# Performance work log

Measured on AMD Instinct MI355X. Metric: run time of the kernel, lower is better.

## Reference

```python
import jax, jax.numpy as jnp
import numpy as np
from functools import partial

H = 1024  # hidden_sz
B, T = 32, 256
NL = 4    # stacked LSTM layers
WSCALE = 0.02


def setup_inputs() -> dict:
    key = jax.random.key(0)
    ks = jax.random.split(key, 8)
    x = jax.random.normal(ks[0], (B, T, H), dtype=jnp.float32)
    h0 = jnp.zeros((B, H), dtype=jnp.float32)
    c0 = jnp.zeros((B, H), dtype=jnp.float32)
    # LSTM params per layer: kernel [H,4H], recurrent kernel [H,4H], bias [4H]
    Wk = jax.random.normal(ks[1], (NL, H, 4 * H), dtype=jnp.float32) * WSCALE
    Wr = jax.random.normal(ks[2], (NL, H, 4 * H), dtype=jnp.float32) * WSCALE
    b = jnp.zeros((NL, 4 * H), dtype=jnp.float32)
    # dense head
    Wd = jax.random.normal(ks[3], (H, H), dtype=jnp.float32) * WSCALE
    bd = jnp.zeros((H,), dtype=jnp.float32)
    return {"x": x, "h0": h0, "c0": c0, "Wk": Wk, "Wr": Wr, "b": b, "Wd": Wd, "bd": bd}


def _lstm_layer(x_tbd, h0, c0, Wk, Wr, b):
    # Keras LSTM with activation='relu', recurrent_activation='sigmoid'.
    # Gate order in keras kernels: i, f, c(candidate), o.
    xw = jnp.einsum('tbd,dg->tbg', x_tbd, Wk) + b  # precompute input projections [T,B,4H]

    def step(carry, xw_t):
        h, c = carry
        z = xw_t + h @ Wr  # [B,4H]
        i, f, g, o = jnp.split(z, 4, axis=-1)
        i = jax.nn.sigmoid(i)
        f = jax.nn.sigmoid(f)
        o = jax.nn.sigmoid(o)
        c = f * c + i * jax.nn.relu(g)
        h = o * jax.nn.relu(c)
        return (h, c), h

    (hT, cT), hs = jax.lax.scan(step, (h0, c0), xw)
    return hs, hT, cT  # hs: [T,B,H]


def reference(x, h0, c0, Wk, Wr, b, Wd, bd):
    # x: [B,T,H] -> time-major [T,B,H]
    seq = jnp.transpose(x, (1, 0, 2))
    h, c = h0, c0
    for l in range(NL):
        seq, h, c = _lstm_layer(seq, h, c, Wk[l], Wr[l], b[l])
        # dropout layers are identity at inference (training=False)
    out = jnp.einsum('tbh,hd->tbd', seq, Wd) + bd
    out = jnp.transpose(out, (1, 0, 2))  # back to [B,T,H]
    return out, h, c
```

## Files before the change

### kernel.cpp

```cpp
#include <hip/hip_runtime.h>

#define TT 256
#define BB 32
#define HH 1024
#define GG 4096

__global__ __launch_bounds__(256) void k_transpose(const float* __restrict__ x, float* __restrict__ seq) {
    int idx = blockIdx.x * 256 + threadIdx.x;
    int k4 = idx & 255;
    int tb = idx >> 8;
    int t = tb >> 5, b = tb & 31;
    float4 v = ((const float4*)x)[((size_t)b * TT + t) * 256 + k4];
    ((float4*)seq)[(size_t)tb * 256 + k4] = v;
}

__global__ __launch_bounds__(256) void k_init_hc(const float* __restrict__ h0, const float* __restrict__ c0,
                                                 float* __restrict__ h, float* __restrict__ c) {
    int i = blockIdx.x * 256 + threadIdx.x;
    ((float4*)h)[i] = ((const float4*)h0)[i];
    ((float4*)c)[i] = ((const float4*)c0)[i];
}

__global__ __launch_bounds__(256) void k_copy_hc(const float* __restrict__ h, const float* __restrict__ c,
                                                 float* __restrict__ oh, float* __restrict__ oc) {
    int i = blockIdx.x * 256 + threadIdx.x;
    ((float4*)oh)[i] = ((const float4*)h)[i];
    ((float4*)oc)[i] = ((const float4*)c)[i];
}

__global__ __launch_bounds__(256) void k_wrt(const float* __restrict__ Wr, float* __restrict__ WrT) {
    __shared__ float tile[64][65];
    int c0 = blockIdx.x * 64;
    int k0 = blockIdx.y * 64;
    int tid = threadIdx.x;
    int tr = tid >> 4, tc4 = tid & 15;
#pragma unroll
    for (int p = 0; p < 4; ++p) {
        int r = p * 16 + tr;
        float4 v = *(const float4*)&Wr[(size_t)(k0 + r) * GG + c0 + tc4 * 4];
        tile[r][tc4 * 4 + 0] = v.x;
        tile[r][tc4 * 4 + 1] = v.y;
        tile[r][tc4 * 4 + 2] = v.z;
        tile[r][tc4 * 4 + 3] = v.w;
    }
    __syncthreads();
#pragma unroll
    for (int p = 0; p < 4; ++p) {
        int cc = p * 16 + tr;
        float4 v;
        v.x = tile[tc4 * 4 + 0][cc];
        v.y = tile[tc4 * 4 + 1][cc];
        v.z = tile[tc4 * 4 + 2][cc];
        v.w = tile[tc4 * 4 + 3][cc];
        *(float4*)&WrT[(size_t)(c0 + cc) * 1024 + k0 + tc4 * 4] = v;
    }
}

template <int MODE>
__global__ __launch_bounds__(256) void k_gemm(const float* __restrict__ A, const float* __restrict__ W,
                                              const float* __restrict__ bias, float* __restrict__ C, int N) {
    __shared__ float As[16][132];
    __shared__ float Bs[16][132];
    const int K = 1024;
    int tid = threadIdx.x;
    int m0 = blockIdx.x * 128, n0 = blockIdx.y * 128;
    int tx = tid & 15, ty = tid >> 4;
    int a_row = tid >> 2, a_kq = tid & 3;
    int b_cq = tid & 31, b_k = tid >> 5;
    float acc[8][8];
#pragma unroll
    for (int i = 0; i < 8; ++i)
#pragma unroll
        for (int jj = 0; jj < 8; ++jj) acc[i][jj] = 0.f;

    for (int kc = 0; kc < K; kc += 16) {
#pragma unroll
        for (int it = 0; it < 2; ++it) {
            int row = a_row + it * 64;
            float4 v = *(const float4*)&A[(size_t)(m0 + row) * K + kc + a_kq * 4];
            As[a_kq * 4 + 0][row] = v.x;
            As[a_kq * 4 + 1][row] = v.y;
            As[a_kq * 4 + 2][row] = v.z;
            As[a_kq * 4 + 3][row] = v.w;
        }
#pragma unroll
        for (int it = 0; it < 2; ++it) {
            int kk = b_k + it * 8;
            float4 v = *(const float4*)&W[(size_t)(kc + kk) * N + n0 + b_cq * 4];
            *(float4*)&Bs[kk][b_cq * 4] = v;
        }
        __syncthreads();
#pragma unroll
        for (int kk = 0; kk < 16; ++kk) {
            float4 a0 = *(const float4*)&As[kk][ty * 8];
            float4 a1 = *(const float4*)&As[kk][ty * 8 + 4];
            float4 b0 = *(const float4*)&Bs[kk][tx * 8];
            float4 b1 = *(const float4*)&Bs[kk][tx * 8 + 4];
            float am[8] = {a0.x, a0.y, a0.z, a0.w, a1.x, a1.y, a1.z, a1.w};
            float bv[8] = {b0.x, b0.y, b0.z, b0.w, b1.x, b1.y, b1.z, b1.w};
#pragma unroll
            for (int i = 0; i < 8; ++i)
#pragma unroll
                for (int jj = 0; jj < 8; ++jj) acc[i][jj] += am[i] * bv[jj];
        }
        __syncthreads();
    }
#pragma unroll
    for (int i = 0; i < 8; ++i) {
        int m = m0 + ty * 8 + i;
#pragma unroll
        for (int jj = 0; jj < 8; jj += 4) {
            int n = n0 + tx * 8 + jj;
            float4 v;
            v.x = acc[i][jj + 0] + bias[n + 0];
            v.y = acc[i][jj + 1] + bias[n + 1];
            v.z = acc[i][jj + 2] + bias[n + 2];
            v.w = acc[i][jj + 3] + bias[n + 3];
            if (MODE == 0) {
                *(float4*)&C[(size_t)m * N + n] = v;
            } else {
                int t = m >> 5, b = m & 31;
                *(float4*)&C[((size_t)b * TT + t) * HH + n] = v;
            }
        }
    }
}

__global__ __launch_bounds__(512) void k_step_T3(const float* __restrict__ WrT, const float* __restrict__ xw_t,
                                                 float* __restrict__ seq_t, const float* __restrict__ h_in,
                                                 float* __restrict__ h_out, float* __restrict__ c) {
    __shared__ float h_lds[34816];
    __shared__ float zred[8][32][17];
    int tid = threadIdx.x;
    int j = tid & 15, ks = tid >> 4;
    int hc0 = blockIdx.x * 4;
    int col = (j >> 2) * HH + hc0 + (j & 3);

    const float4* WrT4 = (const float4*)WrT;
    int wbase = col * 256 + ks * 8;
    float4 w[8];
#pragma unroll
    for (int q = 0; q < 8; ++q) w[q] = WrT4[wbase + q];

    int rb = tid >> 2, rd = tid & 3;
    float pz[4];
    if (tid < 128) {
#pragma unroll
        for (int g = 0; g < 4; ++g) pz[g] = xw_t[rb * GG + g * HH + hc0 + rd];
    }

    const float4* hp4 = (const float4*)h_in;
    float4* hl4w = (float4*)h_lds;
#pragma unroll 8
    for (int it = 0; it < 16; ++it) {
        int gi = it * 512 + tid;
        float4 v = hp4[gi];
        int b = gi >> 8, kk = gi & 255;
        hl4w[b * 272 + (kk >> 4) * 17 + (kk & 15)] = v;
    }
    __syncthreads();

    const float4* hl4 = (const float4*)h_lds;
    int base4 = (ks >> 1) * 17 + (ks & 1) * 8;
    float acc[32];
#pragma unroll
    for (int b = 0; b < 32; ++b) acc[b] = 0.f;
#pragma unroll
    for (int q = 0; q < 8; ++q) {
        float4 wq = w[q];
#pragma unroll
        for (int b = 0; b < 32; ++b) {
            float4 hv = hl4[b * 272 + base4 + q];
            acc[b] += wq.x * hv.x + wq.y * hv.y + wq.z * hv.z + wq.w * hv.w;
        }
    }
#pragma unroll
    for (int b = 0; b < 32; ++b) {
        acc[b] += __shfl_xor(acc[b], 16);
        acc[b] += __shfl_xor(acc[b], 32);
    }
    int wv = tid >> 6;
    if ((ks & 3) == 0) {
#pragma unroll
        for (int b = 0; b < 32; ++b) zred[wv][b][j] = acc[b];
    }
    __syncthreads();

    if (tid < 128) {
        float zz[4];
#pragma unroll
        for (int g = 0; g < 4; ++g) {
            float s = pz[g];
#pragma unroll
            for (int u = 0; u < 8; ++u) s += zred[u][rb][g * 4 + rd];
            zz[g] = s;
        }
        float si = 1.f / (1.f + expf(-zz[0]));
        float sf = 1.f / (1.f + expf(-zz[1]));
        float gg = fmaxf(zz[2], 0.f);
        float so = 1.f / (1.f + expf(-zz[3]));
        float cv = c[rb * HH + hc0 + rd];
        cv = sf * cv + si * gg;
        c[rb * HH + hc0 + rd] = cv;
        float hn = so * fmaxf(cv, 0.f);
        h_out[rb * HH + hc0 + rd] = hn;
        seq_t[rb * HH + hc0 + rd] = hn;
    }
}

__global__ __launch_bounds__(256) void k_step(const float* __restrict__ Wr, const float* __restrict__ xw_t,
                                              float* __restrict__ seq_t, const float* __restrict__ h_in,
                                              float* __restrict__ h_out, float* __restrict__ c) {
    __shared__ float zred[4][32][17];
    int tid = threadIdx.x;
    int j = tid & 15, ks = tid >> 4;
    int hc0 = blockIdx.x * 4;
    int col = (j >> 2) * HH + hc0 + (j & 3);
    float4 w[16];
#pragma unroll
    for (int q = 0; q < 16; ++q) {
        size_t kb = (size_t)(ks * 64 + q * 4) * GG + col;
        w[q].x = Wr[kb];
        w[q].y = Wr[kb + GG];
        w[q].z = Wr[kb + 2 * (size_t)GG];
        w[q].w = Wr[kb + 3 * (size_t)GG];
    }
    const float4* hp = (const float4*)h_in;
    int kq0 = ks * 16;
    float acc[32];
#pragma unroll
    for (int b = 0; b < 32; ++b) acc[b] = 0.f;
#pragma unroll
    for (int q = 0; q < 16; ++q) {
        float4 wq = w[q];
#pragma unroll
        for (int b = 0; b < 32; ++b) {
            float4 hv = hp[b * 256 + kq0 + q];
            acc[b] += wq.x * hv.x + wq.y * hv.y + wq.z * hv.z + wq.w * hv.w;
        }
    }
#pragma unroll
    for (int b = 0; b < 32; ++b) {
        acc[b] += __shfl_xor(acc[b], 16);
        acc[b] += __shfl_xor(acc[b], 32);
    }
    int wv = tid >> 6;
    if ((ks & 3) == 0) {
#pragma unroll
        for (int b = 0; b < 32; ++b) zred[wv][b][j] = acc[b];
    }
    __syncthreads();
    if (tid < 128) {
        int rb = tid >> 2, rd = tid & 3;
        float zz[4];
#pragma unroll
        for (int g = 0; g < 4; ++g) {
            float s = xw_t[rb * GG + g * HH + hc0 + rd];
#pragma unroll
            for (int u = 0; u < 4; ++u) s += zred[u][rb][g * 4 + rd];
            zz[g] = s;
        }
        float si = 1.f / (1.f + expf(-zz[0]));
        float sf = 1.f / (1.f + expf(-zz[1]));
        float gg = fmaxf(zz[2], 0.f);
        float so = 1.f / (1.f + expf(-zz[3]));
        float cv = c[rb * HH + hc0 + rd];
        cv = sf * cv + si * gg;
        c[rb * HH + hc0 + rd] = cv;
        float hn = so * fmaxf(cv, 0.f);
        h_out[rb * HH + hc0 + rd] = hn;
        seq_t[rb * HH + hc0 + rd] = hn;
    }
}

extern "C" void kernel_launch(void* const* d_in, const int* in_sizes, int n_in,
                              void* d_out, int out_size, void* d_ws, size_t ws_size,
                              hipStream_t stream) {
    const float* x  = (const float*)d_in[0];
    const float* h0 = (const float*)d_in[1];
    const float* c0 = (const float*)d_in[2];
    const float* Wk = (const float*)d_in[3];
    const float* Wr = (const float*)d_in[4];
    const float* bs = (const float*)d_in[5];
    const float* Wd = (const float*)d_in[6];
    const float* bd = (const float*)d_in[7];
    float* out = (float*)d_out;
    float* ws  = (float*)d_ws;

    float* xw  = ws;
    float* seq = ws + 33554432;
    float* h0b = seq + 8388608;
    float* h1b = h0b + 32768;
    float* c   = h1b + 32768;
    float* wrt = c + 32768;
    bool fast = ws_size >= (size_t)46235648 * 4;

    k_transpose<<<8192, 256, 0, stream>>>(x, seq);
    k_init_hc<<<32, 256, 0, stream>>>(h0, c0, h0b, c);

    for (int l = 0; l < 4; ++l) {
        const float* Wrl = Wr + (size_t)l * 1024 * 4096;
        k_gemm<0><<<dim3(64, 32), 256, 0, stream>>>(seq, Wk + (size_t)l * 1024 * 4096,
                                                    bs + l * 4096, xw, 4096);
        if (fast) k_wrt<<<dim3(64, 16), 256, 0, stream>>>(Wrl, wrt);
        for (int t = 0; t < TT; ++t) {
            const float* hin = (t & 1) ? h1b : h0b;
            float* hout      = (t & 1) ? h0b : h1b;
            if (fast)
                k_step_T3<<<256, 512, 0, stream>>>(wrt, xw + (size_t)t * (BB * GG),
                                                   seq + (size_t)t * (BB * HH), hin, hout, c);
            else
                k_step<<<256, 256, 0, stream>>>(Wrl, xw + (size_t)t * (BB * GG),
                                                seq + (size_t)t * (BB * HH), hin, hout, c);
        }
    }

    k_gemm<1><<<dim3(64, 8), 256, 0, stream>>>(seq, Wd, bd, out, 1024);
    k_copy_hc<<<32, 256, 0, stream>>>(h0b, c, out + 8388608, out + 8388608 + 32768);
}
```

Measured before the change: 16.56 ms.

## Use split-bf16x3 MFMA GEMM for per-layer input projection

Replaces the FP32 SIMT GEMM for the input projection with an MFMA bf16 GEMM. Both operands are split into three bf16 pieces to emulate FP32 accuracy using six MFMA products. A new kernel transposes and splits Wk each layer into workspace. The aim is to cut the time of the large per-layer projection GEMM, at the cost of extra split/transpose work, more shared memory, and slightly different rounding.

Measured after the change: 14.90 ms. 10.0% less time.

```diff
diff --git a/kernel.cpp b/kernel.cpp
--- a/kernel.cpp
+++ b/kernel.cpp
@@ -4,6 +4,18 @@
 #define BB 32
 #define HH 1024
 #define GG 4096
+
+typedef __attribute__((ext_vector_type(8))) short short8;
+typedef __attribute__((ext_vector_type(4))) float f32x4;
+
+__device__ __forceinline__ unsigned short rne_bf16(float x) {
+    unsigned u = __float_as_uint(x);
+    unsigned r = (u + 0x7FFFu + ((u >> 16) & 1u)) >> 16;
+    return (unsigned short)r;
+}
+__device__ __forceinline__ float bf16f(unsigned short s) {
+    return __uint_as_float((unsigned)s << 16);
+}
 
 __global__ __launch_bounds__(256) void k_transpose(const float* __restrict__ x, float* __restrict__ seq) {
     int idx = blockIdx.x * 256 + threadIdx.x;
@@ -53,6 +65,148 @@
         v.z = tile[tc4 * 4 + 2][cc];
         v.w = tile[tc4 * 4 + 3][cc];
         *(float4*)&WrT[(size_t)(c0 + cc) * 1024 + k0 + tc4 * 4] = v;
+    }
+}
+
+__global__ __launch_bounds__(256) void k_wkt3(const float* __restrict__ Wk, unsigned short* __restrict__ W1,
+                                              unsigned short* __restrict__ W2, unsigned short* __restrict__ W3) {
+    __shared__ float tile[64][65];
+    int c0 = blockIdx.x * 64;
+    int k0 = blockIdx.y * 64;
+    int tid = threadIdx.x;
+    int tr = tid >> 4, tc4 = tid & 15;
+#pragma unroll
+    for (int p = 0; p < 4; ++p) {
+        int r = p * 16 + tr;
+        float4 v = *(const float4*)&Wk[(size_t)(k0 + r) * GG + c0 + tc4 * 4];
+        tile[r][tc4 * 4 + 0] = v.x;
+        tile[r][tc4 * 4 + 1] = v.y;
+        tile[r][tc4 * 4 + 2] = v.z;
+        tile[r][tc4 * 4 + 3] = v.w;
+    }
+    __syncthreads();
+#pragma unroll
+    for (int p = 0; p < 4; ++p) {
+        int cc = p * 16 + tr;
+        ushort4 o1, o2, o3;
+        unsigned short* po1 = (unsigned short*)&o1;
+        unsigned short* po2 = (unsigned short*)&o2;
+        unsigned short* po3 = (unsigned short*)&o3;
+#pragma unroll
+        for (int e = 0; e < 4; ++e) {
+            float v = tile[tc4 * 4 + e][cc];
+            unsigned short s1 = rne_bf16(v);
+            float r1 = v - bf16f(s1);
+            unsigned short s2 = rne_bf16(r1);
+            float r2 = r1 - bf16f(s2);
+            unsigned short s3 = rne_bf16(r2);
+            po1[e] = s1; po2[e] = s2; po3[e] = s3;
+        }
+        size_t off = (size_t)(c0 + cc) * 1024 + k0 + tc4 * 4;
+        *(ushort4*)&W1[off] = o1;
+        *(ushort4*)&W2[off] = o2;
+        *(ushort4*)&W3[off] = o3;
+    }
+}
+
+__global__ __launch_bounds__(256, 2) void k_gemm_mx3(const float* __restrict__ A,
+                                                     const unsigned short* __restrict__ B1,
+                                                     const unsigned short* __restrict__ B2,
+                                                     const unsigned short* __restrict__ B3,
+                                                     const float* __restrict__ bias, float* __restrict__ C) {
+    __shared__ unsigned short Asl[3][6144];
+    __shared__ unsigned short Bsl[3][6144];
+    int tid = threadIdx.x;
+    int m0 = blockIdx.x * 128, n0 = blockIdx.y * 128;
+    int lane = tid & 63, wv = tid >> 6;
+    int wr = (wv >> 1) * 64, wc = (wv & 1) * 64;
+    int l15 = lane & 15, ko = (lane >> 4) * 8;
+
+    f32x4 acc[4][4];
+#pragma unroll
+    for (int i = 0; i < 4; ++i)
+#pragma unroll
+        for (int j = 0; j < 4; ++j) acc[i][j] = (f32x4){0.f, 0.f, 0.f, 0.f};
+
+    const unsigned short* Bg[3] = {B1, B2, B3};
+
+    for (int k0 = 0; k0 < 1024; k0 += 32) {
+#pragma unroll
+        for (int i = 0; i < 4; ++i) {
+            int idx = i * 256 + tid;
+            int m = idx >> 3, kq = idx & 7;
+            float4 v = *(const float4*)&A[(size_t)(m0 + m) * 1024 + k0 + kq * 4];
+            float xs[4] = {v.x, v.y, v.z, v.w};
+            ushort4 o1, o2, o3;
+            unsigned short* po1 = (unsigned short*)&o1;
+            unsigned short* po2 = (unsigned short*)&o2;
+            unsigned short* po3 = (unsigned short*)&o3;
+#pragma unroll
+            for (int e = 0; e < 4; ++e) {
+                unsigned short s1 = rne_bf16(xs[e]);
+                float r1 = xs[e] - bf16f(s1);
+                unsigned short s2 = rne_bf16(r1);
+                float r2 = r1 - bf16f(s2);
+                unsigned short s3 = rne_bf16(r2);
+                po1[e] = s1; po2[e] = s2; po3[e] = s3;
+            }
+            int loff = m * 48 + kq * 4;
+            *(ushort4*)&Asl[0][loff] = o1;
+            *(ushort4*)&Asl[1][loff] = o2;
+            *(ushort4*)&Asl[2][loff] = o3;
+        }
+#pragma unroll
+        for (int sp = 0; sp < 3; ++sp) {
+            const unsigned short* bg = Bg[sp];
+#pragma unroll
+            for (int i = 0; i < 2; ++i) {
+                int idx = i * 256 + tid;
+                int n = idx >> 2, kq = idx & 3;
+                short8 v = *(const short8*)&bg[(size_t)(n0 + n) * 1024 + k0 + kq * 8];
+                *(short8*)&Bsl[sp][n * 48 + kq * 8] = v;
+            }
+        }
+        __syncthreads();
+
+        short8 af[3][4];
+#pragma unroll
+        for (int mi = 0; mi < 4; ++mi) {
+            int ro = (wr + mi * 16 + l15) * 48 + ko;
+#pragma unroll
+            for (int sp = 0; sp < 3; ++sp) af[sp][mi] = *(const short8*)&Asl[sp][ro];
+        }
+#pragma unroll
+        for (int ni = 0; ni < 4; ++ni) {
+            int co = (wc + ni * 16 + l15) * 48 + ko;
+            short8 b0 = *(const short8*)&Bsl[0][co];
+            short8 b1 = *(const short8*)&Bsl[1][co];
+            short8 b2 = *(const short8*)&Bsl[2][co];
+#pragma unroll
+            for (int mi = 0; mi < 4; ++mi) {
+                f32x4 a = acc[mi][ni];
+                a = __builtin_amdgcn_mfma_f32_16x16x32_bf16(af[0][mi], b0, a, 0, 0, 0);
+                a = __builtin_amdgcn_mfma_f32_16x16x32_bf16(af[1][mi], b0, a, 0, 0, 0);
+                a = __builtin_amdgcn_mfma_f32_16x16x32_bf16(af[0][mi], b1, a, 0, 0, 0);
+                a = __builtin_amdgcn_mfma_f32_16x16x32_bf16(af[2][mi], b0, a, 0, 0, 0);
+                a = __builtin_amdgcn_mfma_f32_16x16x32_bf16(af[1][mi], b1, a, 0, 0, 0);
+                a = __builtin_amdgcn_mfma_f32_16x16x32_bf16(af[0][mi], b2, a, 0, 0, 0);
+                acc[mi][ni] = a;
+            }
+        }
+        __syncthreads();
+    }
+
+#pragma unroll
+    for (int ni = 0; ni < 4; ++ni) {
+        int col = n0 + wc + ni * 16 + l15;
+        float bv = bias[col];
+#pragma unroll
+        for (int mi = 0; mi < 4; ++mi) {
+            int rbase = m0 + wr + mi * 16 + (lane >> 4) * 4;
+#pragma unroll
+            for (int r = 0; r < 4; ++r)
+                C[(size_t)(rbase + r) * 4096 + col] = acc[mi][ni][r] + bv;
+        }
     }
 }
 
@@ -293,15 +447,25 @@
     float* h1b = h0b + 32768;
     float* c   = h1b + 32768;
     float* wrt = c + 32768;
-    bool fast = ws_size >= (size_t)46235648 * 4;
+    const size_t base_floats = 46235648;
+    unsigned short* wkt1 = (unsigned short*)(ws + base_floats);
+    unsigned short* wkt2 = wkt1 + 4194304;
+    unsigned short* wkt3 = wkt2 + 4194304;
+    bool fast    = ws_size >= base_floats * 4;
+    bool mfma_ok = ws_size >= base_floats * 4 + (size_t)3 * 4194304 * 2;
 
     k_transpose<<<8192, 256, 0, stream>>>(x, seq);
     k_init_hc<<<32, 256, 0, stream>>>(h0, c0, h0b, c);
 
     for (int l = 0; l < 4; ++l) {
         const float* Wrl = Wr + (size_t)l * 1024 * 4096;
-        k_gemm<0><<<dim3(64, 32), 256, 0, stream>>>(seq, Wk + (size_t)l * 1024 * 4096,
-                                                    bs + l * 4096, xw, 4096);
+        const float* Wkl = Wk + (size_t)l * 1024 * 4096;
+        if (mfma_ok) {
+            k_wkt3<<<dim3(64, 16), 256, 0, stream>>>(Wkl, wkt1, wkt2, wkt3);
+            k_gemm_mx3<<<dim3(64, 32), 256, 0, stream>>>(seq, wkt1, wkt2, wkt3, bs + l * 4096, xw);
+        } else {
+            k_gemm<0><<<dim3(64, 32), 256, 0, stream>>>(seq, Wkl, bs + l * 4096, xw, 4096);
+        }
         if (fast) k_wrt<<<dim3(64, 16), 256, 0, stream>>>(Wrl, wrt);
         for (int t = 0; t < TT; ++t) {
             const float* hin = (t & 1) ? h1b : h0b;
```
